# Kernel optimization log

Measured on AMD Instinct MI355X. Metric: run time of the kernel, lower is better.

The kernel has to match this reference:

```python
import jax, jax.numpy as jnp
import numpy as np

DIM = 2048
N_HEADS = 16
HEAD_DIM = DIM // N_HEADS
SEQ = 1024
BSZ = 2
ADAPTER_LEN = 10
MAX_FEATS = 10
ROPE_THETA = 10000.0


def setup_inputs() -> dict:
    key = jax.random.key(0)
    ks = jax.random.split(key, 10)
    x = jax.random.normal(ks[0], (BSZ, SEQ, DIM), dtype=jnp.float32)
    adapter = jax.random.normal(ks[1], (1, ADAPTER_LEN, DIM), dtype=jnp.float32)
    # causal additive mask [1,1,S,S]
    neg = jnp.full((SEQ, SEQ), -1e9, dtype=jnp.float32)
    mask = jnp.triu(neg, k=1)[None, None]
    # rotary frequencies (real/imag of freqs_cis)
    inv_freq = 1.0 / (ROPE_THETA ** (np.arange(0, HEAD_DIM, 2, dtype=np.float32) / HEAD_DIM))
    t = np.arange(SEQ, dtype=np.float32)
    ang = jnp.asarray(np.outer(t, inv_freq), dtype=jnp.float32)  # [S, HEAD_DIM//2]
    freqs_cos = jnp.cos(ang)
    freqs_sin = jnp.sin(ang)
    scale = 0.02
    wq = jax.random.normal(ks[2], (DIM, DIM), dtype=jnp.float32) * scale
    wk = jax.random.normal(ks[3], (DIM, DIM), dtype=jnp.float32) * scale
    wv = jax.random.normal(ks[4], (DIM, DIM), dtype=jnp.float32) * scale
    wo = jax.random.normal(ks[5], (DIM, DIM), dtype=jnp.float32) * scale
    gate1 = jax.random.normal(ks[6], (1, N_HEADS, 1, 1), dtype=jnp.float32) * 0.5
    gate2 = jnp.ones((1, N_HEADS, 1, 1), dtype=jnp.float32) * -3.0
    return {"x": x, "adapter": adapter, "mask": mask, "freqs_cos": freqs_cos,
            "freqs_sin": freqs_sin, "wq": wq, "wk": wk, "wv": wv, "wo": wo,
            "gate1": gate1, "gate2": gate2, "video_start": 30}


def _apply_rope(t, cos, sin):
    # t: [B,S,H,D]; cos/sin: [S, D//2] -> complex multiply on consecutive pairs
    tr = t.reshape(*t.shape[:-1], HEAD_DIM // 2, 2)
    xr, xi = tr[..., 0], tr[..., 1]
    c = cos[None, :, None, :]
    s = sin[None, :, None, :]
    out_r = xr * c - xi * s
    out_i = xr * s + xi * c
    return jnp.stack([out_r, out_i], axis=-1).reshape(t.shape)


def reference(x, adapter, mask, freqs_cos, freqs_sin, wq, wk, wv, wo, gate1, gate2, video_start):
    bsz, seqlen, _ = x.shape
    al = adapter.shape[1]
    vs = int(video_start)
    # projections (torch Linear: y = x @ W^T)
    xq = (x @ wq.T).reshape(bsz, seqlen, N_HEADS, HEAD_DIM)
    xk = (x @ wk.T).reshape(bsz, seqlen, N_HEADS, HEAD_DIM)
    xv = (x @ wv.T).reshape(bsz, seqlen, N_HEADS, HEAD_DIM)
    xq = _apply_rope(xq, freqs_cos, freqs_sin)
    xk = _apply_rope(xk, freqs_cos, freqs_sin)
    # adapter keys/values (no RoPE), broadcast over batch
    a_k = (adapter @ wk.T).reshape(1, al, N_HEADS, HEAD_DIM)
    a_v = (adapter @ wv.T).reshape(1, al, N_HEADS, HEAD_DIM)
    a_k = jnp.broadcast_to(a_k, (bsz, al, N_HEADS, HEAD_DIM))
    a_v = jnp.broadcast_to(a_v, (bsz, al, N_HEADS, HEAD_DIM))
    keys = jnp.concatenate([a_k, xk], axis=1)      # [B, al+S, H, D]
    values = jnp.concatenate([a_v, xv], axis=1)
    # mask extended with zeros over adapter columns
    extra = jnp.zeros((1, 1, seqlen, al), dtype=mask.dtype)
    full_mask = jnp.concatenate([extra, mask], axis=-1)
    scores = jnp.einsum('bqhd,bkhd->bhqk', xq, keys) / jnp.sqrt(jnp.float32(HEAD_DIM))
    scores = scores + full_mask
    # split softmax: adapter part gated by tanh(gate1)
    adapter_scores = jax.nn.softmax(scores[..., :al], axis=-1) * jnp.tanh(gate1)
    vt = scores[..., al:]
    vt = vt.at[:, :, vs + MAX_FEATS:, vs:vs + MAX_FEATS].add(gate2)
    vt = jax.nn.softmax(vt, axis=-1)
    probs = jnp.concatenate([adapter_scores, vt], axis=-1)  # [B,H,S,al+S]
    out = jnp.einsum('bhqk,bkhd->bqhd', probs, values)
    out = out.reshape(bsz, seqlen, DIM)
    return out @ wo.T
```

## Files before the change

kernel.cpp:

```cpp
#include <hip/hip_runtime.h>
#include <math.h>

#define DIM   2048
#define NH    16
#define HD    128
#define SEQQ  1024
#define BSZ   2
#define AL    10
#define MAXF  10
#define KVROWS (SEQQ + AL)
#define BK    32

typedef unsigned short ushort_t;
typedef __bf16   bf16x8 __attribute__((ext_vector_type(8)));
typedef float    f32x4  __attribute__((ext_vector_type(4)));
typedef ushort_t us8    __attribute__((ext_vector_type(8)));

#define AS1 __attribute__((address_space(1)))
#define AS3 __attribute__((address_space(3)))

__device__ __forceinline__ float b2f(ushort_t u) {
    return __uint_as_float(((unsigned int)u) << 16);
}
__device__ __forceinline__ ushort_t f2b(float f) {
    unsigned int u = __float_as_uint(f);
    u += 0x7fffu + ((u >> 16) & 1u);
    return (ushort_t)(u >> 16);
}
__device__ __forceinline__ float scrub(float v, float canary) {
    return ((__float_as_uint(v) & 0x7f800000u) == 0x7f800000u) ? canary : v;
}
__device__ __forceinline__ bf16x8 cvt8(const float* p) {
    float4 a = *(const float4*)p;
    float4 b = *(const float4*)(p + 4);
    us8 u;
    u[0] = f2b(a.x); u[1] = f2b(a.y); u[2] = f2b(a.z); u[3] = f2b(a.w);
    u[4] = f2b(b.x); u[5] = f2b(b.y); u[6] = f2b(b.z); u[7] = f2b(b.w);
    return *(bf16x8*)&u;
}

__global__ __launch_bounds__(256) void cvt5(
    const float* __restrict__ s0, const float* __restrict__ s1,
    const float* __restrict__ s2, const float* __restrict__ s3,
    const float* __restrict__ s4,
    ushort_t* __restrict__ d0, ushort_t* __restrict__ d1,
    ushort_t* __restrict__ d2, ushort_t* __restrict__ d3,
    ushort_t* __restrict__ d4)
{
    const int y = blockIdx.y;
    const float* s = (y == 0) ? s0 : (y == 1) ? s1 : (y == 2) ? s2 : (y == 3) ? s3 : s4;
    ushort_t*    d = (y == 0) ? d0 : (y == 1) ? d1 : (y == 2) ? d2 : (y == 3) ? d3 : d4;
    size_t i = (size_t)blockIdx.x * 256 + threadIdx.x;
    float4 a = ((const float4*)s)[2 * i];
    float4 b = ((const float4*)s)[2 * i + 1];
    us8 u;
    u[0] = f2b(a.x); u[1] = f2b(a.y); u[2] = f2b(a.z); u[3] = f2b(a.w);
    u[4] = f2b(b.x); u[5] = f2b(b.y); u[6] = f2b(b.z); u[7] = f2b(b.w);
    *(us8*)(d + i * 8) = u;
}

__global__ __launch_bounds__(256) void adapter_gemm(
    const float* __restrict__ adp,
    const ushort_t* __restrict__ Wkb, const ushort_t* __restrict__ Wvb,
    ushort_t* __restrict__ Ko, ushort_t* __restrict__ Vo,
    float canary)
{
    __shared__ ushort_t Al[AL * DIM];

    const int t = threadIdx.x;
    #pragma unroll
    for (int p = 0; p < 10; ++p) {
        int i = p * 256 + t;
        const float* sp = adp + i * 8;
        float4 a = *(const float4*)sp;
        float4 b = *(const float4*)(sp + 4);
        us8 u;
        u[0] = f2b(a.x); u[1] = f2b(a.y); u[2] = f2b(a.z); u[3] = f2b(a.w);
        u[4] = f2b(b.x); u[5] = f2b(b.y); u[6] = f2b(b.z); u[7] = f2b(b.w);
        *(us8*)(Al + i * 8) = u;
    }
    __syncthreads();

    const int z = blockIdx.x >> 8;
    const ushort_t* W = z ? Wvb : Wkb;
    ushort_t*       O = z ? Vo  : Ko;
    const int nbase = (blockIdx.x & 255) * 8;
    const int w = t >> 6, lane = t & 63;

    #pragma unroll
    for (int nn = 0; nn < 2; ++nn) {
        const int n = nbase + w * 2 + nn;
        const ushort_t* wr = W + (size_t)n * DIM;
        float acc[AL] = {};
        #pragma unroll
        for (int c = 0; c < 4; ++c) {
            const int k = c * 512 + lane * 8;
            us8 b8 = *(const us8*)(wr + k);
            float bf[8];
            #pragma unroll
            for (int j = 0; j < 8; ++j) bf[j] = b2f(b8[j]);
            #pragma unroll
            for (int m = 0; m < AL; ++m) {
                us8 a8 = *(const us8*)(Al + m * DIM + k);
                #pragma unroll
                for (int j = 0; j < 8; ++j)
                    acc[m] = fmaf(b2f(a8[j]), bf[j], acc[m]);
            }
        }
        #pragma unroll
        for (int m = 0; m < AL; ++m) {
            float v = acc[m];
            v += __shfl_xor(v, 1);  v += __shfl_xor(v, 2);
            v += __shfl_xor(v, 4);  v += __shfl_xor(v, 8);
            v += __shfl_xor(v, 16); v += __shfl_xor(v, 32);
            if (lane == 0) O[(size_t)m * DIM + n] = f2b(scrub(v, canary));
        }
    }
}

template<bool CF32>
__global__ __launch_bounds__(256) void gemm_bt(
    const ushort_t* __restrict__ A,
    const ushort_t* __restrict__ B0, const ushort_t* __restrict__ B1, const ushort_t* __restrict__ B2,
    void* __restrict__ C0, void* __restrict__ C1, void* __restrict__ C2,
    float canary)
{
    __shared__ ushort_t As[128 * 32];
    __shared__ ushort_t Bs[128 * 32];

    const int z = blockIdx.z;
    const ushort_t* B = (z == 0) ? B0 : (z == 1) ? B1 : B2;
    void*           C = (z == 0) ? C0 : (z == 1) ? C1 : C2;

    const int m0 = blockIdx.y * 128;
    const int n0 = blockIdx.x * 128;
    const int t = threadIdx.x;
    const int w = t >> 6, lane = t & 63;
    const int ln = lane & 15, qd = lane >> 4;
    const int wrow = (w >> 1) * 64, wcol = (w & 1) * 64;

    const int r0 = t >> 2, c0 = (t & 3) * 8;
    const int r1 = (t + 256) >> 2;
    const ushort_t* Ag0 = A + (size_t)(m0 + r0) * DIM + c0;
    const ushort_t* Ag1 = A + (size_t)(m0 + r1) * DIM + c0;
    const ushort_t* Bg0 = B + (size_t)(n0 + r0) * DIM + c0;
    const ushort_t* Bg1 = B + (size_t)(n0 + r1) * DIM + c0;
    ushort_t* Al0 = As + (size_t)t * 8;
    ushort_t* Al1 = As + (size_t)(t + 256) * 8;
    ushort_t* Bl0 = Bs + (size_t)t * 8;
    ushort_t* Bl1 = Bs + (size_t)(t + 256) * 8;

    f32x4 acc[4][4] = {};

    for (int k0 = 0; k0 < DIM; k0 += BK) {
        if (k0) __syncthreads();
        __builtin_amdgcn_global_load_lds((const AS1 void*)(Ag0 + k0), (AS3 void*)Al0, 16, 0, 0);
        __builtin_amdgcn_global_load_lds((const AS1 void*)(Ag1 + k0), (AS3 void*)Al1, 16, 0, 0);
        __builtin_amdgcn_global_load_lds((const AS1 void*)(Bg0 + k0), (AS3 void*)Bl0, 16, 0, 0);
        __builtin_amdgcn_global_load_lds((const AS1 void*)(Bg1 + k0), (AS3 void*)Bl1, 16, 0, 0);
        __syncthreads();

        bf16x8 af[4], bfr[4];
        #pragma unroll
        for (int i = 0; i < 4; ++i) {
            af[i]  = *(const bf16x8*)(As + (wrow + i * 16 + ln) * 32 + qd * 8);
            bfr[i] = *(const bf16x8*)(Bs + (wcol + i * 16 + ln) * 32 + qd * 8);
        }
        #pragma unroll
        for (int i = 0; i < 4; ++i)
            #pragma unroll
            for (int j = 0; j < 4; ++j)
                acc[i][j] = __builtin_amdgcn_mfma_f32_16x16x32_bf16(af[i], bfr[j], acc[i][j], 0, 0, 0);
    }

    #pragma unroll
    for (int i = 0; i < 4; ++i) {
        #pragma unroll
        for (int j = 0; j < 4; ++j) {
            const int gn = n0 + wcol + j * 16 + ln;
            #pragma unroll
            for (int r = 0; r < 4; ++r) {
                const int gm = m0 + wrow + i * 16 + qd * 4 + r;
                float v = scrub(acc[i][j][r], canary);
                if (CF32) ((float*)C)[(size_t)gm * DIM + gn] = v;
                else      ((ushort_t*)C)[(size_t)gm * DIM + gn] = f2b(v);
            }
        }
    }
}

template<bool AF32, bool CF32>
__global__ __launch_bounds__(256) void mfma_gemm(
    const void* __restrict__ Av,
    const float* __restrict__ B0, const float* __restrict__ B1, const float* __restrict__ B2,
    void* __restrict__ C0, void* __restrict__ C1, void* __restrict__ C2,
    int M, float canary)
{
    const int z = blockIdx.z;
    const float* B = (z == 0) ? B0 : (z == 1) ? B1 : B2;
    void*       C = (z == 0) ? C0 : (z == 1) ? C1 : C2;

    const int m0 = blockIdx.y * 128;
    const int n0 = blockIdx.x * 128;
    const int t    = threadIdx.x;
    const int w    = t >> 6;
    const int lane = t & 63;
    const int ln   = lane & 15, qd = lane >> 4;
    const int wrow = (w >> 1) * 64, wcol = (w & 1) * 64;

    size_t aoff[4];
    const float* brow[4];
    #pragma unroll
    for (int i = 0; i < 4; ++i) {
        int gr = m0 + wrow + i * 16 + ln; gr = (gr < M) ? gr : (M - 1);
        aoff[i] = (size_t)gr * DIM + qd * 8;
        brow[i] = B + (size_t)(n0 + wcol + i * 16 + ln) * DIM + qd * 8;
    }

    f32x4 acc[4][4] = {};

    for (int k0 = 0; k0 < DIM; k0 += BK) {
        bf16x8 af[4], bfr[4];
        #pragma unroll
        for (int i = 0; i < 4; ++i) {
            if (AF32) af[i] = cvt8((const float*)Av + aoff[i] + k0);
            else      af[i] = *(const bf16x8*)((const ushort_t*)Av + aoff[i] + k0);
            bfr[i] = cvt8(brow[i] + k0);
        }
        #pragma unroll
        for (int i = 0; i < 4; ++i)
            #pragma unroll
            for (int j = 0; j < 4; ++j)
                acc[i][j] = __builtin_amdgcn_mfma_f32_16x16x32_bf16(af[i], bfr[j], acc[i][j], 0, 0, 0);
    }

    #pragma unroll
    for (int i = 0; i < 4; ++i) {
        #pragma unroll
        for (int j = 0; j < 4; ++j) {
            const int gn = n0 + wcol + j * 16 + ln;
            #pragma unroll
            for (int r = 0; r < 4; ++r) {
                const int gm = m0 + wrow + i * 16 + qd * 4 + r;
                float v = scrub(acc[i][j][r], canary);
                if (gm < M) {
                    if (CF32) ((float*)C)[(size_t)gm * DIM + gn] = v;
                    else      ((ushort_t*)C)[(size_t)gm * DIM + gn] = f2b(v);
                }
            }
        }
    }
}

__global__ __launch_bounds__(256) void rope_kernel(ushort_t* __restrict__ Qb,
                                                   ushort_t* __restrict__ Kb,
                                                   const float* __restrict__ fc,
                                                   const float* __restrict__ fs,
                                                   float qscale)
{
    int i = blockIdx.x * 256 + threadIdx.x;
    ushort_t* T = blockIdx.y ? Kb : Qb;
    const float sc = blockIdx.y ? 1.0f : qscale;
    int row = i >> 10;
    int p   = i & 1023;
    float c = fc[((row & 1023) << 6) + (p & 63)];
    float s = fs[((row & 1023) << 6) + (p & 63)];
    ushort_t* ptr = T + (size_t)row * DIM + p * 2;
    float xr = b2f(ptr[0]), xi = b2f(ptr[1]);
    ptr[0] = f2b((xr * c - xi * s) * sc);
    ptr[1] = f2b((xr * s + xi * c) * sc);
}

__global__ __launch_bounds__(256) void attn_mfma(const ushort_t* __restrict__ Q,
                                                 const ushort_t* __restrict__ Kg,
                                                 const ushort_t* __restrict__ Vg,
                                                 const float* __restrict__ g1,
                                                 const float* __restrict__ g2,
                                                 const int* __restrict__ vsp,
                                                 ushort_t* __restrict__ AO)
{
    __shared__ ushort_t Kls[2][64 * 128];
    __shared__ ushort_t Vt[128 * 72];
    __shared__ ushort_t Pl[4 * 16 * 72];

    const int blk = blockIdx.x;
    const int qt  = 15 - (blk & 15);
    const int h   = (blk >> 4) & 15;
    const int b   = blk >> 8;
    const int q0  = qt * 64;
    const int nsteps = qt + 1;
    const int t = threadIdx.x;
    const int w = t >> 6, lane = t & 63;
    const int ln = lane & 15, g = lane >> 4;
    const int hb = h * HD;
    const size_t kvb = (size_t)b << 10;
    const int vs = *vsp;
    const float g2h = g2[h];
    const float ag  = tanhf(g1[h]);
    const int gq = q0 + w * 16 + ln;

    const ushort_t* qrow = Q + (kvb + gq) * DIM + hb;
    bf16x8 qf[4];
    #pragma unroll
    for (int c = 0; c < 4; ++c) qf[c] = *(const bf16x8*)(qrow + g * 8 + 32 * c);

    const int vk = t & 63, vd0 = (t >> 6) * 8;

    us8 vreg[4];
    {
        const ushort_t* vbase = Vg + (kvb + vk) * DIM + hb;
        #pragma unroll
        for (int p = 0; p < 4; ++p)
            vreg[p] = *(const us8*)(vbase + vd0 + 32 * p);
        #pragma unroll
        for (int p = 0; p < 4; ++p) {
            int i = t + 256 * p;
            int row = i >> 4, slot = (i & 15) ^ (row & 7);
            __builtin_amdgcn_global_load_lds(
                (const AS1 void*)(Kg + (kvb + row) * DIM + hb + slot * 8),
                (AS3 void*)(&Kls[0][i * 8]), 16, 0, 0);
        }
    }

    f32x4 oa[8] = {};
    float m_run = -1e30f, l_run = 0.f;
    ushort_t* Plw = Pl + w * (16 * 72) + ln * 72;

    for (int s = 0; s < nsteps; ++s) {
        const int k0 = s * 64;
        const int cur = s & 1;
        __syncthreads();
        #pragma unroll
        for (int p = 0; p < 4; ++p)
            #pragma unroll
            for (int j = 0; j < 8; ++j)
                Vt[(vd0 + 32 * p + j) * 72 + vk] = vreg[p][j];
        __syncthreads();

        if (s + 1 < nsteps) {
            const ushort_t* vbase = Vg + (kvb + k0 + 64 + vk) * DIM + hb;
            #pragma unroll
            for (int p = 0; p < 4; ++p)
                vreg[p] = *(const us8*)(vbase + vd0 + 32 * p);
            #pragma unroll
            for (int p = 0; p < 4; ++p) {
                int i = t + 256 * p;
                int row = i >> 4, slot = (i & 15) ^ (row & 7);
                __builtin_amdgcn_global_load_lds(
                    (const AS1 void*)(Kg + (kvb + k0 + 64 + row) * DIM + hb + slot * 8),
                    (AS3 void*)(&Kls[cur ^ 1][i * 8]), 16, 0, 0);
            }
        }

        f32x4 sc[4] = {};
        #pragma unroll
        for (int mt = 0; mt < 4; ++mt) {
            const int krow = ln + 16 * mt;
            const ushort_t* krp = &Kls[cur][krow * 128];
            #pragma unroll
            for (int c = 0; c < 4; ++c) {
                bf16x8 kf = *(const bf16x8*)(krp + ((8 * g + 32 * c) ^ ((krow & 7) << 3)));
                sc[mt] = __builtin_amdgcn_mfma_f32_16x16x32_bf16(kf, qf[c], sc[mt], 0, 0, 0);
            }
        }

        float mloc = -3e38f;
        #pragma unroll
        for (int mt = 0; mt < 4; ++mt)
            #pragma unroll
            for (int r = 0; r < 4; ++r) {
                int gk = k0 + mt * 16 + g * 4 + r;
                float v = sc[mt][r];
                if (gk > gq) v -= 1e9f;
                if (gk >= vs && gk < vs + MAXF && gq >= vs + MAXF) v += g2h;
                sc[mt][r] = v;
                mloc = fmaxf(mloc, v);
            }
        mloc = fmaxf(mloc, __shfl_xor(mloc, 16));
        mloc = fmaxf(mloc, __shfl_xor(mloc, 32));
        const float m_new = fmaxf(m_run, mloc);
        const float alpha = __expf(m_run - m_new);
        float psum = 0.f;
        #pragma unroll
        for (int mt = 0; mt < 4; ++mt) {
            float p0 = __expf(sc[mt][0] - m_new);
            float p1 = __expf(sc[mt][1] - m_new);
            float p2 = __expf(sc[mt][2] - m_new);
            float p3 = __expf(sc[mt][3] - m_new);
            psum += (p0 + p1) + (p2 + p3);
            uint2 pw_;
            pw_.x = (unsigned)f2b(p0) | ((unsigned)f2b(p1) << 16);
            pw_.y = (unsigned)f2b(p2) | ((unsigned)f2b(p3) << 16);
            *(uint2*)(Plw + mt * 16 + g * 4) = pw_;
        }
        psum += __shfl_xor(psum, 16);
        psum += __shfl_xor(psum, 32);
        l_run = l_run * alpha + psum;
        m_run = m_new;
        #pragma unroll
        for (int i = 0; i < 8; ++i) {
            oa[i][0] *= alpha; oa[i][1] *= alpha; oa[i][2] *= alpha; oa[i][3] *= alpha;
        }

        bf16x8 pf0 = *(const bf16x8*)(Plw + 8 * g);
        bf16x8 pf1 = *(const bf16x8*)(Plw + 32 + 8 * g);
        #pragma unroll
        for (int dt = 0; dt < 8; ++dt) {
            const ushort_t* vrp = &Vt[(dt * 16 + ln) * 72];
            bf16x8 vf0 = *(const bf16x8*)(vrp + 8 * g);
            bf16x8 vf1 = *(const bf16x8*)(vrp + 32 + 8 * g);
            oa[dt] = __builtin_amdgcn_mfma_f32_16x16x32_bf16(vf0, pf0, oa[dt], 0, 0, 0);
            oa[dt] = __builtin_amdgcn_mfma_f32_16x16x32_bf16(vf1, pf1, oa[dt], 0, 0, 0);
        }
    }

    const float invl = 1.f / l_run;
    #pragma unroll
    for (int i = 0; i < 8; ++i) {
        oa[i][0] *= invl; oa[i][1] *= invl; oa[i][2] *= invl; oa[i][3] *= invl;
    }

    __syncthreads();
    if ((t >> 4) < 10) {
        int ak = t >> 4, adc = t & 15;
        us8 av = *(const us8*)(Vg + (size_t)(2048 + ak) * DIM + hb + adc * 8);
        #pragma unroll
        for (int j = 0; j < 8; ++j)
            Vt[(adc * 8 + j) * 72 + ak] = av[j];
    }
    __syncthreads();

    const ushort_t* karow = Kg + (size_t)(2048 + (ln < 10 ? ln : 9)) * DIM + hb;
    f32x4 sa4 = {};
    #pragma unroll
    for (int c = 0; c < 4; ++c) {
        bf16x8 kf = *(const bf16x8*)(karow + 8 * g + 32 * c);
        sa4 = __builtin_amdgcn_mfma_f32_16x16x32_bf16(kf, qf[c], sa4, 0, 0, 0);
    }
    float am = -3e38f;
    float pa[4];
    #pragma unroll
    for (int r = 0; r < 4; ++r) {
        int kl = g * 4 + r;
        pa[r] = (kl < 10) ? sa4[r] : -1e30f;
        am = fmaxf(am, pa[r]);
    }
    am = fmaxf(am, __shfl_xor(am, 16));
    am = fmaxf(am, __shfl_xor(am, 32));
    float asum = 0.f;
    #pragma unroll
    for (int r = 0; r < 4; ++r) { pa[r] = __expf(pa[r] - am); asum += pa[r]; }
    asum += __shfl_xor(asum, 16);
    asum += __shfl_xor(asum, 32);
    const float coef = ag / asum;
    {
        uint2 pw_;
        pw_.x = (unsigned)f2b(pa[0] * coef) | ((unsigned)f2b(pa[1] * coef) << 16);
        pw_.y = (unsigned)f2b(pa[2] * coef) | ((unsigned)f2b(pa[3] * coef) << 16);
        *(uint2*)(Plw + g * 4) = pw_;
        uint2 z2; z2.x = 0; z2.y = 0;
        *(uint2*)(Plw + 16 + g * 4) = z2;
    }
    bf16x8 paf = *(const bf16x8*)(Plw + 8 * g);
    #pragma unroll
    for (int dt = 0; dt < 8; ++dt) {
        const ushort_t* vrp = &Vt[(dt * 16 + ln) * 72];
        bf16x8 vf0 = *(const bf16x8*)(vrp + 8 * g);
        oa[dt] = __builtin_amdgcn_mfma_f32_16x16x32_bf16(vf0, paf, oa[dt], 0, 0, 0);
    }

    ushort_t* outp = AO + (kvb + gq) * DIM + hb;
    #pragma unroll
    for (int dt = 0; dt < 8; ++dt) {
        ushort4 ov;
        ov.x = f2b(scrub(oa[dt][0], 1e8f));
        ov.y = f2b(scrub(oa[dt][1], 1e8f));
        ov.z = f2b(scrub(oa[dt][2], 1e8f));
        ov.w = f2b(scrub(oa[dt][3], 1e8f));
        *(ushort4*)(outp + dt * 16 + g * 4) = ov;
    }
}

__global__ __launch_bounds__(256) void attn_kernel(const ushort_t* __restrict__ Q,
                                                   const ushort_t* __restrict__ Kg,
                                                   const ushort_t* __restrict__ Vg,
                                                   const float* __restrict__ g1,
                                                   const float* __restrict__ g2,
                                                   const int* __restrict__ vsp,
                                                   ushort_t* __restrict__ AO)
{
    __shared__ float Qs[32 * 132];
    __shared__ float Ks[32 * 132];
    __shared__ float Vs[32 * 132];
    __shared__ float Ps[32 * 32];

    const int blk = blockIdx.x;
    const int q0  = (31 - (blk & 31)) * 32;
    const int h   = blk >> 5;
    const int t   = threadIdx.x;
    const int qi  = t >> 3;
    const int l8  = t & 7;
    const int vs  = *vsp;
    const int g_q = q0 + qi;
    const float scale = 0.08838834764831845f;
    const float g2h = g2[h];
    const float ag  = tanhf(g1[h]);

    #pragma unroll
    for (int p = 0; p < 4; ++p) {
        int idx = (p * 256 + t) * 4;
        int r = idx >> 7, d = idx & 127;
        ushort4 q4 = *(const ushort4*)(Q + (size_t)(q0 + r) * DIM + h * HD + d);
        *(float4*)(Qs + r * 132 + d) = make_float4(b2f(q4.x), b2f(q4.y), b2f(q4.z), b2f(q4.w));
    }

    float o[16];
    #pragma unroll
    for (int i = 0; i < 16; ++i) o[i] = 0.f;
    float m_run = -1e30f, l_run = 0.f;

    for (int k0 = 0; k0 <= q0 + 31; k0 += 32) {
        __syncthreads();
        #pragma unroll
        for (int p = 0; p < 4; ++p) {
            int idx = (p * 256 + t) * 4;
            int r = idx >> 7, d = idx & 127;
            size_t goff = (size_t)(k0 + r) * DIM + h * HD + d;
            ushort4 k4 = *(const ushort4*)(Kg + goff);
            ushort4 v4 = *(const ushort4*)(Vg + goff);
            *(float4*)(Ks + r * 132 + d) = make_float4(b2f(k4.x), b2f(k4.y), b2f(k4.z), b2f(k4.w));
            *(float4*)(Vs + r * 132 + d) = make_float4(b2f(v4.x), b2f(v4.y), b2f(v4.z), b2f(v4.w));
        }
        __syncthreads();

        float s[4];
        #pragma unroll
        for (int jj = 0; jj < 4; ++jj) s[jj] = 0.f;
        #pragma unroll 4
        for (int d = 0; d < 128; d += 4) {
            const float4 qv = *(const float4*)(Qs + qi * 132 + d);
            #pragma unroll
            for (int jj = 0; jj < 4; ++jj) {
                const float4 kv = *(const float4*)(Ks + (l8 + 8 * jj) * 132 + d);
                s[jj] += qv.x * kv.x + qv.y * kv.y + qv.z * kv.z + qv.w * kv.w;
            }
        }
        float mloc = -1e30f;
        #pragma unroll
        for (int jj = 0; jj < 4; ++jj) {
            int gk = k0 + l8 + 8 * jj;
            float sv = s[jj] * scale;
            if (gk > g_q) sv -= 1e9f;
            if (gk >= vs && gk < vs + MAXF && g_q >= vs + MAXF) sv += g2h;
            s[jj] = sv;
            mloc = fmaxf(mloc, sv);
        }
        mloc = fmaxf(mloc, __shfl_xor(mloc, 1));
        mloc = fmaxf(mloc, __shfl_xor(mloc, 2));
        mloc = fmaxf(mloc, __shfl_xor(mloc, 4));
        const float m_new = fmaxf(m_run, mloc);
        const float alpha = expf(m_run - m_new);
        float psum = 0.f;
        #pragma unroll
        for (int jj = 0; jj < 4; ++jj) {
            float pv = expf(s[jj] - m_new);
            psum += pv;
            Ps[qi * 32 + l8 + 8 * jj] = pv;
        }
        psum += __shfl_xor(psum, 1);
        psum += __shfl_xor(psum, 2);
        psum += __shfl_xor(psum, 4);
        l_run = l_run * alpha + psum;
        m_run = m_new;
        #pragma unroll
        for (int i = 0; i < 16; ++i) o[i] *= alpha;
        __syncthreads();

        #pragma unroll 4
        for (int kk = 0; kk < 32; ++kk) {
            const float pp = Ps[qi * 32 + kk];
            const float* vr = Vs + kk * 132 + l8 * 4;
            #pragma unroll
            for (int jj = 0; jj < 4; ++jj) {
                const float4 v4 = *(const float4*)(vr + jj * 32);
                o[jj*4+0] = fmaf(pp, v4.x, o[jj*4+0]);
                o[jj*4+1] = fmaf(pp, v4.y, o[jj*4+1]);
                o[jj*4+2] = fmaf(pp, v4.z, o[jj*4+2]);
                o[jj*4+3] = fmaf(pp, v4.w, o[jj*4+3]);
            }
        }
    }

    const float invl = 1.f / l_run;
    #pragma unroll
    for (int i = 0; i < 16; ++i) o[i] *= invl;

    __syncthreads();
    #pragma unroll
    for (int p = 0; p < 2; ++p) {
        int idx = p * 256 + t;
        if (idx < 320) {
            int fi = idx * 4; int r = fi >> 7; int d = fi & 127;
            size_t goff = (size_t)(SEQQ + r) * DIM + h * HD + d;
            ushort4 k4 = *(const ushort4*)(Kg + goff);
            ushort4 v4 = *(const ushort4*)(Vg + goff);
            *(float4*)(Ks + r * 132 + d) = make_float4(b2f(k4.x), b2f(k4.y), b2f(k4.z), b2f(k4.w));
            *(float4*)(Vs + r * 132 + d) = make_float4(b2f(v4.x), b2f(v4.y), b2f(v4.z), b2f(v4.w));
        }
    }
    __syncthreads();
    float sa[2] = {-1e30f, -1e30f};
    #pragma unroll
    for (int jj = 0; jj < 2; ++jj) {
        int kk = l8 + 8 * jj;
        if (kk < AL) {
            float acc = 0.f;
            #pragma unroll 4
            for (int d = 0; d < 128; d += 4) {
                const float4 qv = *(const float4*)(Qs + qi * 132 + d);
                const float4 kv = *(const float4*)(Ks + kk * 132 + d);
                acc += qv.x * kv.x + qv.y * kv.y + qv.z * kv.z + qv.w * kv.w;
            }
            sa[jj] = acc * scale;
        }
    }
    float am = fmaxf(sa[0], sa[1]);
    am = fmaxf(am, __shfl_xor(am, 1));
    am = fmaxf(am, __shfl_xor(am, 2));
    am = fmaxf(am, __shfl_xor(am, 4));
    float pa0 = expf(sa[0] - am);
    float pa1 = (l8 < 2) ? expf(sa[1] - am) : 0.f;
    float asum = pa0 + pa1;
    asum += __shfl_xor(asum, 1);
    asum += __shfl_xor(asum, 2);
    asum += __shfl_xor(asum, 4);
    const float coef = ag / asum;
    Ps[qi * 32 + l8] = pa0 * coef;
    if (l8 < 2) Ps[qi * 32 + 8 + l8] = pa1 * coef;
    __syncthreads();
    #pragma unroll
    for (int kk = 0; kk < AL; ++kk) {
        const float pp = Ps[qi * 32 + kk];
        const float* vr = Vs + kk * 132 + l8 * 4;
        #pragma unroll
        for (int jj = 0; jj < 4; ++jj) {
            const float4 v4 = *(const float4*)(vr + jj * 32);
            o[jj*4+0] = fmaf(pp, v4.x, o[jj*4+0]);
            o[jj*4+1] = fmaf(pp, v4.y, o[jj*4+1]);
            o[jj*4+2] = fmaf(pp, v4.z, o[jj*4+2]);
            o[jj*4+3] = fmaf(pp, v4.w, o[jj*4+3]);
        }
    }

    ushort_t* outp = AO + (size_t)g_q * DIM + h * HD + l8 * 4;
    #pragma unroll
    for (int jj = 0; jj < 4; ++jj) {
        ushort4 ov;
        ov.x = f2b(scrub(o[jj*4+0], 1e8f));
        ov.y = f2b(scrub(o[jj*4+1], 1e8f));
        ov.z = f2b(scrub(o[jj*4+2], 1e8f));
        ov.w = f2b(scrub(o[jj*4+3], 1e8f));
        *(ushort4*)(outp + jj * 32) = ov;
    }
}

extern "C" void kernel_launch(void* const* d_in, const int* in_sizes, int n_in,
                              void* d_out, int out_size, void* d_ws, size_t ws_size,
                              hipStream_t stream)
{
    const float* x   = (const float*)d_in[0];
    const float* adp = (const float*)d_in[1];
    const float* fc  = (const float*)d_in[3];
    const float* fs  = (const float*)d_in[4];
    const float* wq  = (const float*)d_in[5];
    const float* wk  = (const float*)d_in[6];
    const float* wv  = (const float*)d_in[7];
    const float* wo  = (const float*)d_in[8];
    const float* g1  = (const float*)d_in[9];
    const float* g2  = (const float*)d_in[10];
    const int*   vsp = (const int*)d_in[11];

    float* out = (float*)d_out;

    const size_t rows2 = (size_t)BSZ * SEQQ;
    const size_t qe2 = rows2 * DIM;
    const size_t ke2 = (rows2 + AL) * DIM;
    const size_t we  = (size_t)DIM * DIM;
    const size_t xe  = (size_t)BSZ * SEQQ * DIM;
    const size_t need = (qe2 + 2 * ke2 + xe + 4 * we) * sizeof(ushort_t);

    if (ws_size >= need) {
        ushort_t* Qb  = (ushort_t*)d_ws;
        ushort_t* Kb  = Qb + qe2;
        ushort_t* Vb  = Kb + ke2;
        ushort_t* Xb  = Vb + ke2;
        ushort_t* Wqb = Xb + xe;
        ushort_t* Wkb = Wqb + we;
        ushort_t* Wvb = Wkb + we;
        ushort_t* Wob = Wvb + we;

        cvt5<<<dim3(2048, 5), 256, 0, stream>>>(wq, wk, wv, wo, x,
                                                Wqb, Wkb, Wvb, Wob, Xb);

        adapter_gemm<<<512, 256, 0, stream>>>(adp, Wkb, Wvb,
                                              Kb + rows2 * DIM, Vb + rows2 * DIM,
                                              100.0f);

        gemm_bt<false><<<dim3(16, 16, 3), 256, 0, stream>>>(
            Xb, Wqb, Wkb, Wvb, Qb, Kb, Vb, 1e5f);

        rope_kernel<<<dim3(8192, 2), 256, 0, stream>>>(Qb, Kb, fc, fs,
                                                       0.08838834764831845f);

        attn_mfma<<<512, 256, 0, stream>>>(Qb, Kb, Vb, g1, g2, vsp, Qb );

        gemm_bt<true><<<dim3(16, 16, 1), 256, 0, stream>>>(
            Qb, Wob, Wob, Wob, out, out, out, 1e12f);
    } else {
        const size_t qe = (size_t)SEQQ * DIM;
        const size_t ke = (size_t)KVROWS * DIM;
        ushort_t* Qb = (ushort_t*)d_ws;
        ushort_t* Kb = Qb + qe;
        ushort_t* Vb = Kb + ke;

        mfma_gemm<true, false><<<dim3(16, 1, 2), 256, 0, stream>>>(
            adp, wk, wv, wv,
            Kb + qe, Vb + qe, Vb,
            AL, 100.0f);

        for (int b = 0; b < BSZ; ++b) {
            const long xo = (long)b * SEQQ * DIM;
            mfma_gemm<true, false><<<dim3(16, 8, 3), 256, 0, stream>>>(
                x + xo, wq, wk, wv, Qb, Kb, Vb, SEQQ, 1e5f);

            rope_kernel<<<dim3(4096, 2), 256, 0, stream>>>(Qb, Kb, fc, fs, 1.0f);

            attn_kernel<<<NH * (SEQQ / 32), 256, 0, stream>>>(Qb, Kb, Vb, g1, g2, vsp, Qb);

            mfma_gemm<false, true><<<dim3(16, 8, 1), 256, 0, stream>>>(
                Qb, wo, wo, wo, out + xo, out + xo, out + xo, SEQQ, 1e12f);
        }
    }
}
```

Before: 310.0 us.

## Store V transposed from projection GEMM and stage it via async LDS loads

The V projection epilogue now writes V transposed into a padded global buffer (per-feature rows of length VTP), with the adapter V values and zero padding appended by the adapter kernel. The attention kernel then double-buffers both K and V tiles with global_load_lds using an XOR swizzle, dropping the register-held V prefetch, the per-step LDS transpose scatter, and one barrier per step. Block-to-tile mapping is also remapped to interleave long and short causal q-tiles across XCDs for load balance. This costs strided transposed writes in the GEMM epilogue and a larger workspace.

```diff
diff --git a/kernel.cpp b/kernel.cpp
--- a/kernel.cpp
+++ b/kernel.cpp
@@ -10,6 +10,7 @@
 #define MAXF  10
 #define KVROWS (SEQQ + AL)
 #define BK    32
+#define VTP   2080
 
 typedef unsigned short ushort_t;
 typedef __bf16   bf16x8 __attribute__((ext_vector_type(8)));
@@ -62,7 +63,7 @@
 __global__ __launch_bounds__(256) void adapter_gemm(
     const float* __restrict__ adp,
     const ushort_t* __restrict__ Wkb, const ushort_t* __restrict__ Wvb,
-    ushort_t* __restrict__ Ko, ushort_t* __restrict__ Vo,
+    ushort_t* __restrict__ Ko, ushort_t* __restrict__ VtO,
     float canary)
 {
     __shared__ ushort_t Al[AL * DIM];
@@ -83,7 +84,6 @@
 
     const int z = blockIdx.x >> 8;
     const ushort_t* W = z ? Wvb : Wkb;
-    ushort_t*       O = z ? Vo  : Ko;
     const int nbase = (blockIdx.x & 255) * 8;
     const int w = t >> 6, lane = t & 63;
 
@@ -113,12 +113,17 @@
             v += __shfl_xor(v, 1);  v += __shfl_xor(v, 2);
             v += __shfl_xor(v, 4);  v += __shfl_xor(v, 8);
             v += __shfl_xor(v, 16); v += __shfl_xor(v, 32);
-            if (lane == 0) O[(size_t)m * DIM + n] = f2b(scrub(v, canary));
-        }
-    }
-}
-
-template<bool CF32>
+            if (lane == 0) {
+                ushort_t ov = f2b(scrub(v, canary));
+                if (z) VtO[(size_t)n * VTP + 2048 + m] = ov;
+                else   Ko[(size_t)m * DIM + n] = ov;
+            }
+        }
+        if (z && lane < 22) VtO[(size_t)n * VTP + 2058 + lane] = 0;
+    }
+}
+
+template<int MODE>
 __global__ __launch_bounds__(256) void gemm_bt(
     const ushort_t* __restrict__ A,
     const ushort_t* __restrict__ B0, const ushort_t* __restrict__ B1, const ushort_t* __restrict__ B2,
@@ -178,12 +183,21 @@
         #pragma unroll
         for (int j = 0; j < 4; ++j) {
             const int gn = n0 + wcol + j * 16 + ln;
-            #pragma unroll
-            for (int r = 0; r < 4; ++r) {
-                const int gm = m0 + wrow + i * 16 + qd * 4 + r;
-                float v = scrub(acc[i][j][r], canary);
-                if (CF32) ((float*)C)[(size_t)gm * DIM + gn] = v;
-                else      ((ushort_t*)C)[(size_t)gm * DIM + gn] = f2b(v);
+            const int gm0 = m0 + wrow + i * 16 + qd * 4;
+            if (MODE == 0 && z == 2) {
+                ushort4 ov;
+                ov.x = f2b(scrub(acc[i][j][0], canary));
+                ov.y = f2b(scrub(acc[i][j][1], canary));
+                ov.z = f2b(scrub(acc[i][j][2], canary));
+                ov.w = f2b(scrub(acc[i][j][3], canary));
+                *(ushort4*)((ushort_t*)C + (size_t)gn * VTP + gm0) = ov;
+            } else {
+                #pragma unroll
+                for (int r = 0; r < 4; ++r) {
+                    float v = scrub(acc[i][j][r], canary);
+                    if (MODE == 1) ((float*)C)[(size_t)(gm0 + r) * DIM + gn] = v;
+                    else           ((ushort_t*)C)[(size_t)(gm0 + r) * DIM + gn] = f2b(v);
+                }
             }
         }
     }
@@ -273,20 +287,23 @@
 
 __global__ __launch_bounds__(256) void attn_mfma(const ushort_t* __restrict__ Q,
                                                  const ushort_t* __restrict__ Kg,
-                                                 const ushort_t* __restrict__ Vg,
+                                                 const ushort_t* __restrict__ Vt,
                                                  const float* __restrict__ g1,
                                                  const float* __restrict__ g2,
                                                  const int* __restrict__ vsp,
                                                  ushort_t* __restrict__ AO)
 {
     __shared__ ushort_t Kls[2][64 * 128];
-    __shared__ ushort_t Vt[128 * 72];
+    __shared__ ushort_t Vls[2][128 * 64];
     __shared__ ushort_t Pl[4 * 16 * 72];
 
     const int blk = blockIdx.x;
-    const int qt  = 15 - (blk & 15);
-    const int h   = (blk >> 4) & 15;
-    const int b   = blk >> 8;
+    const int wg   = (blk & 7) * 64 + (blk >> 3);
+    const int gidx = wg >> 4;
+    const int mem  = wg & 15;
+    const int qt   = (mem & 1) ? (mem >> 1) : (15 - (mem >> 1));
+    const int h = gidx & 15;
+    const int b = gidx >> 4;
     const int q0  = qt * 64;
     const int nsteps = qt + 1;
     const int t = threadIdx.x;
@@ -304,23 +321,26 @@
     #pragma unroll
     for (int c = 0; c < 4; ++c) qf[c] = *(const bf16x8*)(qrow + g * 8 + 32 * c);
 
-    const int vk = t & 63, vd0 = (t >> 6) * 8;
-
-    us8 vreg[4];
-    {
-        const ushort_t* vbase = Vg + (kvb + vk) * DIM + hb;
-        #pragma unroll
-        for (int p = 0; p < 4; ++p)
-            vreg[p] = *(const us8*)(vbase + vd0 + 32 * p);
+    auto stage = [&](int bi, int k0) {
         #pragma unroll
         for (int p = 0; p < 4; ++p) {
             int i = t + 256 * p;
-            int row = i >> 4, slot = (i & 15) ^ (row & 7);
+            int kr = i >> 4, ks = (i & 15) ^ (kr & 7);
             __builtin_amdgcn_global_load_lds(
-                (const AS1 void*)(Kg + (kvb + row) * DIM + hb + slot * 8),
-                (AS3 void*)(&Kls[0][i * 8]), 16, 0, 0);
-        }
-    }
+                (const AS1 void*)(Kg + (kvb + k0 + kr) * DIM + hb + ks * 8),
+                (AS3 void*)(&Kls[bi][i * 8]), 16, 0, 0);
+        }
+        #pragma unroll
+        for (int p = 0; p < 4; ++p) {
+            int i = t + 256 * p;
+            int vr = i >> 3, vsl = (i & 7) ^ (vr & 7);
+            __builtin_amdgcn_global_load_lds(
+                (const AS1 void*)(Vt + (size_t)(hb + vr) * VTP + kvb + k0 + vsl * 8),
+                (AS3 void*)(&Vls[bi][i * 8]), 16, 0, 0);
+        }
+    };
+
+    stage(0, 0);
 
     f32x4 oa[8] = {};
     float m_run = -1e30f, l_run = 0.f;
@@ -330,27 +350,7 @@
         const int k0 = s * 64;
         const int cur = s & 1;
         __syncthreads();
-        #pragma unroll
-        for (int p = 0; p < 4; ++p)
-            #pragma unroll
-            for (int j = 0; j < 8; ++j)
-                Vt[(vd0 + 32 * p + j) * 72 + vk] = vreg[p][j];
-        __syncthreads();
-
-        if (s + 1 < nsteps) {
-            const ushort_t* vbase = Vg + (kvb + k0 + 64 + vk) * DIM + hb;
-            #pragma unroll
-            for (int p = 0; p < 4; ++p)
-                vreg[p] = *(const us8*)(vbase + vd0 + 32 * p);
-            #pragma unroll
-            for (int p = 0; p < 4; ++p) {
-                int i = t + 256 * p;
-                int row = i >> 4, slot = (i & 15) ^ (row & 7);
-                __builtin_amdgcn_global_load_lds(
-                    (const AS1 void*)(Kg + (kvb + k0 + 64 + row) * DIM + hb + slot * 8),
-                    (AS3 void*)(&Kls[cur ^ 1][i * 8]), 16, 0, 0);
-            }
-        }
+        if (s + 1 < nsteps) stage(cur ^ 1, k0 + 64);
 
         f32x4 sc[4] = {};
         #pragma unroll
@@ -406,9 +406,10 @@
         bf16x8 pf1 = *(const bf16x8*)(Plw + 32 + 8 * g);
         #pragma unroll
         for (int dt = 0; dt < 8; ++dt) {
-            const ushort_t* vrp = &Vt[(dt * 16 + ln) * 72];
-            bf16x8 vf0 = *(const bf16x8*)(vrp + 8 * g);
-            bf16x8 vf1 = *(const bf16x8*)(vrp + 32 + 8 * g);
+            const int vrow = dt * 16 + ln;
+            const ushort_t* vrp = &Vls[cur][vrow * 64];
+            bf16x8 vf0 = *(const bf16x8*)(vrp + ((g     ^ (vrow & 7)) * 8));
+            bf16x8 vf1 = *(const bf16x8*)(vrp + (((g+4) ^ (vrow & 7)) * 8));
             oa[dt] = __builtin_amdgcn_mfma_f32_16x16x32_bf16(vf0, pf0, oa[dt], 0, 0, 0);
             oa[dt] = __builtin_amdgcn_mfma_f32_16x16x32_bf16(vf1, pf1, oa[dt], 0, 0, 0);
         }
@@ -419,16 +420,6 @@
     for (int i = 0; i < 8; ++i) {
         oa[i][0] *= invl; oa[i][1] *= invl; oa[i][2] *= invl; oa[i][3] *= invl;
     }
-
-    __syncthreads();
-    if ((t >> 4) < 10) {
-        int ak = t >> 4, adc = t & 15;
-        us8 av = *(const us8*)(Vg + (size_t)(2048 + ak) * DIM + hb + adc * 8);
-        #pragma unroll
-        for (int j = 0; j < 8; ++j)
-            Vt[(adc * 8 + j) * 72 + ak] = av[j];
-    }
-    __syncthreads();
 
     const ushort_t* karow = Kg + (size_t)(2048 + (ln < 10 ? ln : 9)) * DIM + hb;
     f32x4 sa4 = {};
@@ -464,9 +455,9 @@
     bf16x8 paf = *(const bf16x8*)(Plw + 8 * g);
     #pragma unroll
     for (int dt = 0; dt < 8; ++dt) {
-        const ushort_t* vrp = &Vt[(dt * 16 + ln) * 72];
-        bf16x8 vf0 = *(const bf16x8*)(vrp + 8 * g);
-        oa[dt] = __builtin_amdgcn_mfma_f32_16x16x32_bf16(vf0, paf, oa[dt], 0, 0, 0);
+        const ushort_t* varow = Vt + (size_t)(hb + dt * 16 + ln) * VTP + 2048;
+        bf16x8 vfa = *(const bf16x8*)(varow + 8 * g);
+        oa[dt] = __builtin_amdgcn_mfma_f32_16x16x32_bf16(vfa, paf, oa[dt], 0, 0, 0);
     }
 
     ushort_t* outp = AO + (kvb + gq) * DIM + hb;
@@ -685,15 +676,16 @@
     const size_t rows2 = (size_t)BSZ * SEQQ;
     const size_t qe2 = rows2 * DIM;
     const size_t ke2 = (rows2 + AL) * DIM;
+    const size_t vte = (size_t)DIM * VTP;
     const size_t we  = (size_t)DIM * DIM;
     const size_t xe  = (size_t)BSZ * SEQQ * DIM;
-    const size_t need = (qe2 + 2 * ke2 + xe + 4 * we) * sizeof(ushort_t);
+    const size_t need = (qe2 + ke2 + vte + xe + 4 * we) * sizeof(ushort_t);
 
     if (ws_size >= need) {
         ushort_t* Qb  = (ushort_t*)d_ws;
         ushort_t* Kb  = Qb + qe2;
-        ushort_t* Vb  = Kb + ke2;
-        ushort_t* Xb  = Vb + ke2;
+        ushort_t* VtG = Kb + ke2;
+        ushort_t* Xb  = VtG + vte;
         ushort_t* Wqb = Xb + xe;
         ushort_t* Wkb = Wqb + we;
         ushort_t* Wvb = Wkb + we;
@@ -703,18 +695,18 @@
                                                 Wqb, Wkb, Wvb, Wob, Xb);
 
         adapter_gemm<<<512, 256, 0, stream>>>(adp, Wkb, Wvb,
-                                              Kb + rows2 * DIM, Vb + rows2 * DIM,
+                                              Kb + rows2 * DIM, VtG,
                                               100.0f);
 
-        gemm_bt<false><<<dim3(16, 16, 3), 256, 0, stream>>>(
-            Xb, Wqb, Wkb, Wvb, Qb, Kb, Vb, 1e5f);
+        gemm_bt<0><<<dim3(16, 16, 3), 256, 0, stream>>>(
+            Xb, Wqb, Wkb, Wvb, Qb, Kb, VtG, 1e5f);
 
         rope_kernel<<<dim3(8192, 2), 256, 0, stream>>>(Qb, Kb, fc, fs,
                                                        0.08838834764831845f);
 
-        attn_mfma<<<512, 256, 0, stream>>>(Qb, Kb, Vb, g1, g2, vsp, Qb );
-
-        gemm_bt<true><<<dim3(16, 16, 1), 256, 0, stream>>>(
+        attn_mfma<<<512, 256, 0, stream>>>(Qb, Kb, VtG, g1, g2, vsp, Qb );
+
+        gemm_bt<1><<<dim3(16, 16, 1), 256, 0, stream>>>(
             Qb, Wob, Wob, Wob, out, out, out, 1e12f);
     } else {
         const size_t qe = (size_t)SEQQ * DIM;
```

Measured after the change: 302.6 us. 2.4% less time.
